# Kernel tuning notes

Hardware: AMD Instinct MI355X
Metric: run time of the kernel (lower is better)

## Reference

```python
import jax, jax.numpy as jnp
import numpy as np

DEPTH = 6


def sparsemax_last(z):
    # sparsemax along the last axis (Martins & Astudillo 2016)
    z_sorted = jnp.sort(z, axis=-1)[..., ::-1]
    k = jnp.arange(1, z.shape[-1] + 1, dtype=z.dtype)
    z_cum = jnp.cumsum(z_sorted, axis=-1)
    support = (1.0 + k * z_sorted) > z_cum
    k_z = jnp.sum(support, axis=-1, keepdims=True)  # number of support elems
    tau = (jnp.take_along_axis(z_cum, k_z.astype(jnp.int32) - 1, axis=-1) - 1.0) / k_z.astype(z.dtype)
    return jnp.maximum(z - tau, 0.0)


def binary_lookup_table(depth):
    # (depth, 2^depth, 2): bit d of leaf index c, stacked with its complement
    indices = np.arange(2 ** depth)
    offsets = 2 ** np.arange(depth)
    bits = (indices[None, :] // offsets[:, None]) % 2
    lut = np.stack([bits, 1 - bits], axis=-1).astype(np.float32)
    return jnp.asarray(lut)


def setup_inputs() -> dict:
    key = jax.random.key(0)
    k1, k2, k3 = jax.random.split(key, 3)
    batch, dim, n_trees, depth, units = 8192, 128, 512, DEPTH, 8
    inputs = jax.random.normal(k1, (batch, dim), dtype=jnp.float32)
    feature_selection_logits = jax.random.uniform(k2, (dim, n_trees, depth), dtype=jnp.float32)
    feature_thresholds = jnp.ones((n_trees, depth), dtype=jnp.float32)
    log_temperatures = jnp.ones((n_trees, depth), dtype=jnp.float32)
    response = jax.random.uniform(k3, (n_trees, units, 2 ** depth), dtype=jnp.float32)
    return {
        "inputs": inputs,
        "feature_selection_logits": feature_selection_logits,
        "feature_thresholds": feature_thresholds,
        "log_temperatures": log_temperatures,
        "response": response,
    }


def reference(inputs, feature_selection_logits, feature_thresholds, log_temperatures, response):
    depth = feature_thresholds.shape[-1]
    lut = binary_lookup_table(depth)  # (depth, C, 2)

    # sparsemax feature selection over the input-feature axis (dim)
    # logits: (dim, n, d) -> (n, d, dim)
    sel = sparsemax_last(jnp.transpose(feature_selection_logits, (1, 2, 0)))
    feature_values = jnp.einsum('bi,ndi->bnd', inputs, sel)  # (b, n, d)

    tl = (feature_values - feature_thresholds) * jnp.exp(-log_temperatures)
    gates = jnp.clip(0.5 * jnp.stack([-tl, tl], axis=-1) + 0.5, 0.0, 1.0)  # (b, n, d, 2)

    # leaf aggregation: prod over depth of per-level LUT contraction.
    # Loop over tiny depth axis to avoid materializing (b, n, d, 2^d).
    agg = None
    for i in range(depth):
        level = jnp.einsum('bns,cs->bnc', gates[:, :, i, :], lut[i])  # (b, n, C)
        agg = level if agg is None else agg * level

    out = jnp.einsum('bnc,nuc->bnu', agg, response)  # (b, n, units)
    return jnp.mean(out, axis=1)  # (b, units)
```

## Files before the change

### kernel.cpp

```cpp
#include <hip/hip_runtime.h>
#include <math.h>

#define BATCH  8192
#define DIM    128
#define NTREES 512
#define UNITS  8
#define RB 64
#define TB 64
#define NROWBLK (BATCH/RB)
#define NTREEBLK (NTREES/TB)

typedef __attribute__((ext_vector_type(8))) __bf16 bf16x8;
typedef __attribute__((ext_vector_type(4))) float f32x4;
typedef __attribute__((ext_vector_type(2))) float f32x2;
typedef __attribute__((ext_vector_type(4))) unsigned int u32x4;

static __device__ inline unsigned short f2bf(float v) {
  __bf16 h = (__bf16)v;
  return *(unsigned short*)&h;
}

static __device__ inline unsigned cvtpk(f32x2 v) {
  unsigned r;
  asm("v_cvt_pk_bf16_f32 %0, %1, %2" : "=v"(r) : "v"(v[0]), "v"(v[1]));
  return r;
}

__global__ __launch_bounds__(128) void prep_all(
    const float* __restrict__ logits, const float* __restrict__ thr,
    const float* __restrict__ logtemp, const float* __restrict__ inputs,
    const float* __restrict__ resp,
    unsigned short* __restrict__ Wfrag, unsigned short* __restrict__ Ximg,
    unsigned short* __restrict__ Rb, float* __restrict__ biasPad)
{
  const int b = blockIdx.x, tid = threadIdx.x;
  if (b < 4096) {
    const int t = b >> 3, d = b & 7;
    const int tb = t >> 6, sub = (t >> 4) & 3, w = (t >> 2) & 3, tq = t & 3;
    const int p = d >> 2, dloc = d & 3;
    const int ln = tq * 4 + dloc;
    const int S = (tb * 4 + sub) * 4 + w;
    const int ks = tid >> 5, G = (tid >> 3) & 3, j = tid & 7;
    const int lane = G * 16 + ln;
    const size_t wi = ((size_t)((S * 2 + p) * 4 + ks) * 64 + lane) * 8 + j;
    if (d >= 6) {
      Wfrag[wi] = 0;
      if (tid == 0) biasPad[t * 8 + d] = 0.f;
      return;
    }
    __shared__ __align__(16) float z[128];
    __shared__ float rc[128], rs[128];
    float zi = logits[((size_t)tid * NTREES + t) * 6 + d];
    z[tid] = zi;
    __syncthreads();
    float k = 0.f, Ssum = 0.f;
    const float4* z4 = (const float4*)z;
    #pragma unroll 4
    for (int q = 0; q < 32; ++q) {
      float4 v = z4[q];
      if (v.x >= zi) { k += 1.f; Ssum += v.x; }
      if (v.y >= zi) { k += 1.f; Ssum += v.y; }
      if (v.z >= zi) { k += 1.f; Ssum += v.z; }
      if (v.w >= zi) { k += 1.f; Ssum += v.w; }
    }
    bool sup = (1.f + k * zi) > Ssum;
    rc[tid] = sup ? 1.f : 0.f;
    rs[tid] = sup ? zi : 0.f;
    __syncthreads();
    for (int off = 64; off > 0; off >>= 1) {
      if (tid < off) { rc[tid] += rc[tid + off]; rs[tid] += rs[tid + off]; }
      __syncthreads();
    }
    float tau = (rs[0] - 1.f) / rc[0];
    float et = expf(-logtemp[t*6 + d]);
    Wfrag[wi] = f2bf(fmaxf(zi - tau, 0.f) * et);
    if (tid == 0) biasPad[t*8 + d] = -thr[t*6 + d] * et;
  } else if (b < 12288) {
    const int r = b - 4096;
    float v = inputs[(size_t)r * DIM + tid];
    int col = ((tid * 2) ^ ((r & 7) << 4)) >> 1;
    Ximg[(size_t)r * DIM + col] = f2bf(v);
  } else {
    const int idx = (b - 12288) * 128 + tid;
    const int j = idx & 7, lane = (idx >> 3) & 63;
    const int ks = (idx >> 9) & 3, half = (idx >> 11) & 1, S = idx >> 12;
    const int G = lane >> 4, u = lane & 15;
    const int tree = S * 4 + G;
    const int leaf = j | (ks << 3) | (half << 5);
    float v = (u < UNITS) ? resp[((size_t)tree*UNITS + u)*64 + leaf] : 0.f;
    Rb[idx] = f2bf(v);
  }
}

__global__ __launch_bounds__(256, 3) void odt_main(
    const unsigned short* __restrict__ Ximg, const unsigned short* __restrict__ Wfrag,
    const float* __restrict__ biasPad, const unsigned short* __restrict__ Rb,
    float* __restrict__ partial)
{
  __shared__ __align__(16) char pool[18432];
  char* Xl = pool;
  float* biasl = (float*)(pool + 16384);
  float* outred = (float*)pool;

  const int tid = threadIdx.x;
  const int lane = tid & 63;
  const int w = tid >> 6;
  const int G = lane >> 4;
  const int ln = lane & 15;

  const int wg = blockIdx.x;
  const int tb = wg & 7;
  const int bx = wg >> 3;

  {
    const float4* src = (const float4*)(Ximg + (size_t)bx * RB * DIM);
    float4* dst = (float4*)Xl;
    #pragma unroll
    for (int it = 0; it < 4; ++it) dst[tid + it * 256] = src[tid + it * 256];
  }
  biasl[tid]       = biasPad[(size_t)tb * 512 + tid];
  biasl[tid + 256] = biasPad[(size_t)tb * 512 + 256 + tid];
  __syncthreads();

  const char* xbase[4];
  #pragma unroll
  for (int ks = 0; ks < 4; ++ks)
    xbase[ks] = Xl + ln*256 + ((ks*64 + G*16) ^ ((ln & 7) << 4));

  f32x4 out[4];
  #pragma unroll
  for (int nt = 0; nt < 4; ++nt)
    #pragma unroll
    for (int r = 0; r < 4; ++r) out[nt][r] = 0.f;

  #pragma unroll 1
  for (int sub = 0; sub < 4; ++sub) {
    const int S = (tb*4 + sub)*4 + w;
    const bf16x8* wf = (const bf16x8*)Wfrag + (size_t)S * 8 * 64;
    const bf16x8* rb = (const bf16x8*)Rb   + (size_t)S * 8 * 64;
    bf16x8 Afr[2][4], B2[2][4];
    #pragma unroll
    for (int p = 0; p < 2; ++p)
      #pragma unroll
      for (int ks = 0; ks < 4; ++ks) {
        Afr[p][ks] = wf[(p*4 + ks)*64 + lane];
        B2[p][ks]  = rb[(p*4 + ks)*64 + lane];
      }
    const int tl8 = (sub*16 + w*4 + G) * 8;
    f32x2 bb[6];
    #pragma unroll
    for (int d = 0; d < 6; ++d) {
      float bvd = biasl[tl8 + d];
      bb[d] = (f32x2){0.5f + 0.5f*bvd, 0.5f - 0.5f*bvd};
    }

    #pragma unroll
    for (int nt = 0; nt < 4; ++nt) {
      bf16x8 Bfr[4];
      #pragma unroll
      for (int ks = 0; ks < 4; ++ks)
        Bfr[ks] = *(const bf16x8*)(xbase[ks] + nt*4096);
      f32x4 c1[2];
      #pragma unroll
      for (int p = 0; p < 2; ++p)
        #pragma unroll
        for (int r = 0; r < 4; ++r) c1[p][r] = 0.f;
      #pragma unroll
      for (int ks = 0; ks < 4; ++ks)
        c1[0] = __builtin_amdgcn_mfma_f32_16x16x32_bf16(Afr[0][ks], Bfr[ks], c1[0], 0,0,0);
      #pragma unroll
      for (int ks = 0; ks < 4; ++ks)
        c1[1] = __builtin_amdgcn_mfma_f32_16x16x32_bf16(Afr[1][ks], Bfr[ks], c1[1], 0,0,0);

      const f32x2 ch = (f32x2){0.5f, -0.5f};
      f32x2 P[6];
      #pragma unroll
      for (int d = 0; d < 6; ++d) {
        float fdv = (d < 4) ? c1[0][d] : c1[1][d-4];
        f32x2 t = fdv*ch + bb[d];
        P[d] = __builtin_elementwise_min(
                 __builtin_elementwise_max(t, (f32x2)0.f), (f32x2)1.f);
      }
      f32x2 qA = P[0]*P[1][0], qB = P[0]*P[1][1];
      f32x2 p3a = qA*P[2][0], p3b = qB*P[2][0];
      f32x2 p3c = qA*P[2][1], p3d = qB*P[2][1];
      f32x2 c34A = P[3]*P[4][0];
      f32x2 c34B = P[3]*P[4][1];

      #pragma unroll
      for (int h = 0; h < 2; ++h) {
        f32x2 ccA = c34A*P[5][h], ccB = c34B*P[5][h];
        float cc[4] = { ccA[0], ccA[1], ccB[0], ccB[1] };
        #pragma unroll
        for (int ks = 0; ks < 4; ++ks) {
          float c = cc[ks];
          u32x4 aw;
          aw[0] = cvtpk(p3a*c);
          aw[1] = cvtpk(p3b*c);
          aw[2] = cvtpk(p3c*c);
          aw[3] = cvtpk(p3d*c);
          bf16x8 A = __builtin_bit_cast(bf16x8, aw);
          out[nt] = __builtin_amdgcn_mfma_f32_16x16x32_bf16(A, B2[h][ks], out[nt], 0,0,0);
        }
      }
    }
  }

  __syncthreads();
  if (ln < UNITS) {
    #pragma unroll
    for (int nt = 0; nt < 4; ++nt)
      #pragma unroll
      for (int r = 0; r < 4; ++r)
        outred[((size_t)w*64 + nt*16 + 4*G + r)*8 + ln] = out[nt][r];
  }
  __syncthreads();
  #pragma unroll
  for (int v = 0; v < 2; ++v) {
    int e = tid + v*256;
    int row = e >> 3, u = e & 7;
    float sum = outred[(0*64 + row)*8 + u]
              + outred[(1*64 + row)*8 + u]
              + outred[(2*64 + row)*8 + u]
              + outred[(3*64 + row)*8 + u];
    partial[((size_t)tb*BATCH + bx*RB + row)*8 + u] = sum;
  }
}

__global__ __launch_bounds__(256) void odt_reduce(
    const f32x4* __restrict__ partial, f32x4* __restrict__ out)
{
  int i = blockIdx.x*256 + threadIdx.x;
  f32x4 sv;
  #pragma unroll
  for (int r = 0; r < 4; ++r) sv[r] = 0.f;
  #pragma unroll
  for (int t = 0; t < NTREEBLK; ++t) {
    f32x4 v = partial[(size_t)t * (BATCH*UNITS/4) + i];
    #pragma unroll
    for (int r = 0; r < 4; ++r) sv[r] += v[r];
  }
  #pragma unroll
  for (int r = 0; r < 4; ++r) sv[r] *= (1.f/NTREES);
  out[i] = sv;
}

extern "C" void kernel_launch(void* const* d_in, const int* in_sizes, int n_in,
                              void* d_out, int out_size, void* d_ws, size_t ws_size,
                              hipStream_t stream)
{
  const float* inputs   = (const float*)d_in[0];
  const float* logits   = (const float*)d_in[1];
  const float* thr      = (const float*)d_in[2];
  const float* logtemp  = (const float*)d_in[3];
  const float* response = (const float*)d_in[4];
  float* out = (float*)d_out;

  char* ws = (char*)d_ws;
  unsigned short* Wfrag = (unsigned short*)(ws);
  unsigned short* Ximg  = (unsigned short*)(ws + (1<<20));
  unsigned short* Rb    = (unsigned short*)(ws + (3<<20));
  float* biasPad        = (float*)(ws + (4<<20));
  float* partial        = (float*)(ws + (4<<20) + (1<<14));

  hipLaunchKernelGGL(prep_all, dim3(16384), dim3(128), 0, stream,
                     logits, thr, logtemp, inputs, response,
                     Wfrag, Ximg, Rb, biasPad);
  hipLaunchKernelGGL(odt_main, dim3(NROWBLK * NTREEBLK), dim3(256), 0, stream,
                     Ximg, Wfrag, biasPad, Rb, partial);
  hipLaunchKernelGGL(odt_reduce, dim3(BATCH * UNITS / 4 / 256), dim3(256), 0, stream,
                     (const f32x4*)partial, (f32x4*)out);
}
```

Measured before the change: 47.12 us.

## Split row tiles into two passes to cut registers and raise occupancy

The main kernel now processes the four 16-row tiles in two passes of two. Each pass keeps only two output accumulators and loads the response fragments later, which lowers live registers so launch bounds can target 4 waves per SIMD instead of 3. The cost is that the weight fragments and response fragments are reloaded from global memory twice per sub-block, plus an extra LDS reduction round per pass in a separate LDS region. Within each pass, the first-stage MFMAs for both tiles are grouped before the gating math, which gives the scheduler more overlap.

Result: slower. 48.34 us (+2.6%).

```diff
diff --git a/kernel.cpp b/kernel.cpp
--- a/kernel.cpp
+++ b/kernel.cpp
@@ -92,15 +92,15 @@
   }
 }
 
-__global__ __launch_bounds__(256, 3) void odt_main(
+__global__ __launch_bounds__(256, 4) void odt_main(
     const unsigned short* __restrict__ Ximg, const unsigned short* __restrict__ Wfrag,
     const float* __restrict__ biasPad, const unsigned short* __restrict__ Rb,
     float* __restrict__ partial)
 {
-  __shared__ __align__(16) char pool[18432];
+  __shared__ __align__(16) char pool[22528];
   char* Xl = pool;
   float* biasl = (float*)(pool + 16384);
-  float* outred = (float*)pool;
+  float* red   = (float*)(pool + 18432);
 
   const int tid = threadIdx.x;
   const int lane = tid & 63;
@@ -127,103 +127,114 @@
   for (int ks = 0; ks < 4; ++ks)
     xbase[ks] = Xl + ln*256 + ((ks*64 + G*16) ^ ((ln & 7) << 4));
 
-  f32x4 out[4];
-  #pragma unroll
-  for (int nt = 0; nt < 4; ++nt)
+  const f32x2 ch = (f32x2){0.5f, -0.5f};
+
+  #pragma unroll 1
+  for (int ntp = 0; ntp < 2; ++ntp) {
+    f32x4 out[2];
     #pragma unroll
-    for (int r = 0; r < 4; ++r) out[nt][r] = 0.f;
-
-  #pragma unroll 1
-  for (int sub = 0; sub < 4; ++sub) {
-    const int S = (tb*4 + sub)*4 + w;
-    const bf16x8* wf = (const bf16x8*)Wfrag + (size_t)S * 8 * 64;
-    const bf16x8* rb = (const bf16x8*)Rb   + (size_t)S * 8 * 64;
-    bf16x8 Afr[2][4], B2[2][4];
-    #pragma unroll
-    for (int p = 0; p < 2; ++p)
-      #pragma unroll
-      for (int ks = 0; ks < 4; ++ks) {
-        Afr[p][ks] = wf[(p*4 + ks)*64 + lane];
-        B2[p][ks]  = rb[(p*4 + ks)*64 + lane];
+    for (int n2 = 0; n2 < 2; ++n2)
+      #pragma unroll
+      for (int r = 0; r < 4; ++r) out[n2][r] = 0.f;
+
+    #pragma unroll 1
+    for (int sub = 0; sub < 4; ++sub) {
+      const int S = (tb*4 + sub)*4 + w;
+      const bf16x8* wf = (const bf16x8*)Wfrag + (size_t)S * 8 * 64;
+      const bf16x8* rb = (const bf16x8*)Rb   + (size_t)S * 8 * 64;
+
+      bf16x8 Afr[2][4];
+      #pragma unroll
+      for (int p = 0; p < 2; ++p)
+        #pragma unroll
+        for (int ks = 0; ks < 4; ++ks)
+          Afr[p][ks] = wf[(p*4 + ks)*64 + lane];
+
+      f32x4 c1[2][2];
+      #pragma unroll
+      for (int n2 = 0; n2 < 2; ++n2) {
+        const int nt = ntp*2 + n2;
+        bf16x8 Bfr[4];
+        #pragma unroll
+        for (int ks = 0; ks < 4; ++ks)
+          Bfr[ks] = *(const bf16x8*)(xbase[ks] + nt*4096);
+        #pragma unroll
+        for (int p = 0; p < 2; ++p)
+          #pragma unroll
+          for (int r = 0; r < 4; ++r) c1[n2][p][r] = 0.f;
+        #pragma unroll
+        for (int ks = 0; ks < 4; ++ks)
+          c1[n2][0] = __builtin_amdgcn_mfma_f32_16x16x32_bf16(Afr[0][ks], Bfr[ks], c1[n2][0], 0,0,0);
+        #pragma unroll
+        for (int ks = 0; ks < 4; ++ks)
+          c1[n2][1] = __builtin_amdgcn_mfma_f32_16x16x32_bf16(Afr[1][ks], Bfr[ks], c1[n2][1], 0,0,0);
       }
-    const int tl8 = (sub*16 + w*4 + G) * 8;
-    f32x2 bb[6];
-    #pragma unroll
-    for (int d = 0; d < 6; ++d) {
-      float bvd = biasl[tl8 + d];
-      bb[d] = (f32x2){0.5f + 0.5f*bvd, 0.5f - 0.5f*bvd};
-    }
-
-    #pragma unroll
-    for (int nt = 0; nt < 4; ++nt) {
-      bf16x8 Bfr[4];
-      #pragma unroll
-      for (int ks = 0; ks < 4; ++ks)
-        Bfr[ks] = *(const bf16x8*)(xbase[ks] + nt*4096);
-      f32x4 c1[2];
-      #pragma unroll
-      for (int p = 0; p < 2; ++p)
-        #pragma unroll
-        for (int r = 0; r < 4; ++r) c1[p][r] = 0.f;
-      #pragma unroll
-      for (int ks = 0; ks < 4; ++ks)
-        c1[0] = __builtin_amdgcn_mfma_f32_16x16x32_bf16(Afr[0][ks], Bfr[ks], c1[0], 0,0,0);
-      #pragma unroll
-      for (int ks = 0; ks < 4; ++ks)
-        c1[1] = __builtin_amdgcn_mfma_f32_16x16x32_bf16(Afr[1][ks], Bfr[ks], c1[1], 0,0,0);
-
-      const f32x2 ch = (f32x2){0.5f, -0.5f};
-      f32x2 P[6];
+
+      bf16x8 B2[2][4];
+      #pragma unroll
+      for (int h = 0; h < 2; ++h)
+        #pragma unroll
+        for (int ks = 0; ks < 4; ++ks)
+          B2[h][ks] = rb[(h*4 + ks)*64 + lane];
+
+      const int tl8 = (sub*16 + w*4 + G) * 8;
+      f32x2 bb[6];
       #pragma unroll
       for (int d = 0; d < 6; ++d) {
-        float fdv = (d < 4) ? c1[0][d] : c1[1][d-4];
-        f32x2 t = fdv*ch + bb[d];
-        P[d] = __builtin_elementwise_min(
-                 __builtin_elementwise_max(t, (f32x2)0.f), (f32x2)1.f);
+        float bvd = biasl[tl8 + d];
+        bb[d] = (f32x2){0.5f + 0.5f*bvd, 0.5f - 0.5f*bvd};
       }
-      f32x2 qA = P[0]*P[1][0], qB = P[0]*P[1][1];
-      f32x2 p3a = qA*P[2][0], p3b = qB*P[2][0];
-      f32x2 p3c = qA*P[2][1], p3d = qB*P[2][1];
-      f32x2 c34A = P[3]*P[4][0];
-      f32x2 c34B = P[3]*P[4][1];
-
-      #pragma unroll
-      for (int h = 0; h < 2; ++h) {
-        f32x2 ccA = c34A*P[5][h], ccB = c34B*P[5][h];
-        float cc[4] = { ccA[0], ccA[1], ccB[0], ccB[1] };
-        #pragma unroll
-        for (int ks = 0; ks < 4; ++ks) {
-          float c = cc[ks];
-          u32x4 aw;
-          aw[0] = cvtpk(p3a*c);
-          aw[1] = cvtpk(p3b*c);
-          aw[2] = cvtpk(p3c*c);
-          aw[3] = cvtpk(p3d*c);
-          bf16x8 A = __builtin_bit_cast(bf16x8, aw);
-          out[nt] = __builtin_amdgcn_mfma_f32_16x16x32_bf16(A, B2[h][ks], out[nt], 0,0,0);
+
+      #pragma unroll
+      for (int n2 = 0; n2 < 2; ++n2) {
+        f32x2 P[6];
+        #pragma unroll
+        for (int d = 0; d < 6; ++d) {
+          float fdv = (d < 4) ? c1[n2][0][d] : c1[n2][1][d-4];
+          f32x2 t = fdv*ch + bb[d];
+          P[d] = __builtin_elementwise_min(
+                   __builtin_elementwise_max(t, (f32x2)0.f), (f32x2)1.f);
+        }
+        f32x2 qA = P[0]*P[1][0], qB = P[0]*P[1][1];
+        f32x2 p3a = qA*P[2][0], p3b = qB*P[2][0];
+        f32x2 p3c = qA*P[2][1], p3d = qB*P[2][1];
+        f32x2 c34A = P[3]*P[4][0];
+        f32x2 c34B = P[3]*P[4][1];
+
+        #pragma unroll
+        for (int h = 0; h < 2; ++h) {
+          f32x2 ccA = c34A*P[5][h], ccB = c34B*P[5][h];
+          float cc[4] = { ccA[0], ccA[1], ccB[0], ccB[1] };
+          #pragma unroll
+          for (int ks = 0; ks < 4; ++ks) {
+            float c = cc[ks];
+            u32x4 aw;
+            aw[0] = cvtpk(p3a*c);
+            aw[1] = cvtpk(p3b*c);
+            aw[2] = cvtpk(p3c*c);
+            aw[3] = cvtpk(p3d*c);
+            bf16x8 A = __builtin_bit_cast(bf16x8, aw);
+            out[n2] = __builtin_amdgcn_mfma_f32_16x16x32_bf16(A, B2[h][ks], out[n2], 0,0,0);
+          }
         }
       }
     }
-  }
-
-  __syncthreads();
-  if (ln < UNITS) {
-    #pragma unroll
-    for (int nt = 0; nt < 4; ++nt)
-      #pragma unroll
-      for (int r = 0; r < 4; ++r)
-        outred[((size_t)w*64 + nt*16 + 4*G + r)*8 + ln] = out[nt][r];
-  }
-  __syncthreads();
-  #pragma unroll
-  for (int v = 0; v < 2; ++v) {
-    int e = tid + v*256;
-    int row = e >> 3, u = e & 7;
-    float sum = outred[(0*64 + row)*8 + u]
-              + outred[(1*64 + row)*8 + u]
-              + outred[(2*64 + row)*8 + u]
-              + outred[(3*64 + row)*8 + u];
-    partial[((size_t)tb*BATCH + bx*RB + row)*8 + u] = sum;
+
+    __syncthreads();
+    if (ln < UNITS) {
+      #pragma unroll
+      for (int n2 = 0; n2 < 2; ++n2)
+        #pragma unroll
+        for (int r = 0; r < 4; ++r)
+          red[w*256 + (n2*16 + 4*G + r)*8 + ln] = out[n2][r];
+    }
+    __syncthreads();
+    {
+      int row = tid >> 3, u = tid & 7;
+      float sum = red[0*256 + tid] + red[1*256 + tid]
+                + red[2*256 + tid] + red[3*256 + tid];
+      partial[((size_t)tb*BATCH + bx*RB + ntp*32 + row)*8 + u] = sum;
+    }
   }
 }
 
```

## Fuse input bf16 conversion into main kernel and compact padded weight/response fragments

Applied to the files above, without the earlier changes.

Drops the separate prep pass that converted inputs to a swizzled bf16 image. The main kernel now loads fp32 inputs directly, packs them to bf16 and writes the swizzled layout into LDS. The Wfrag and Rb fragment layouts are also compacted so the zero-padded depth rows and unused unit lanes are no longer written or stored, which shrinks the prep grid and the preprocessing traffic. In exchange, every odt_main workgroup re-reads fp32 inputs (twice the bytes of bf16) and converts them once per tree block, and the fragment loads use duplicated lane indexing.

Result: slower. 49.51 us (+5.1%).

```diff
diff --git a/kernel.cpp b/kernel.cpp
--- a/kernel.cpp
+++ b/kernel.cpp
@@ -9,11 +9,13 @@
 #define TB 64
 #define NROWBLK (BATCH/RB)
 #define NTREEBLK (NTREES/TB)
+#define WP1BASE 262144
 
 typedef __attribute__((ext_vector_type(8))) __bf16 bf16x8;
 typedef __attribute__((ext_vector_type(4))) float f32x4;
 typedef __attribute__((ext_vector_type(2))) float f32x2;
 typedef __attribute__((ext_vector_type(4))) unsigned int u32x4;
+typedef __attribute__((ext_vector_type(2))) unsigned int u32x2;
 
 static __device__ inline unsigned short f2bf(float v) {
   __bf16 h = (__bf16)v;
@@ -28,25 +30,23 @@
 
 __global__ __launch_bounds__(128) void prep_all(
     const float* __restrict__ logits, const float* __restrict__ thr,
-    const float* __restrict__ logtemp, const float* __restrict__ inputs,
-    const float* __restrict__ resp,
-    unsigned short* __restrict__ Wfrag, unsigned short* __restrict__ Ximg,
-    unsigned short* __restrict__ Rb, float* __restrict__ biasPad)
+    const float* __restrict__ logtemp, const float* __restrict__ resp,
+    unsigned short* __restrict__ Wfrag, unsigned short* __restrict__ Rb,
+    float* __restrict__ biasPad)
 {
   const int b = blockIdx.x, tid = threadIdx.x;
   if (b < 4096) {
     const int t = b >> 3, d = b & 7;
+    if (d >= 6) return;
     const int tb = t >> 6, sub = (t >> 4) & 3, w = (t >> 2) & 3, tq = t & 3;
-    const int p = d >> 2, dloc = d & 3;
-    const int ln = tq * 4 + dloc;
     const int S = (tb * 4 + sub) * 4 + w;
     const int ks = tid >> 5, G = (tid >> 3) & 3, j = tid & 7;
-    const int lane = G * 16 + ln;
-    const size_t wi = ((size_t)((S * 2 + p) * 4 + ks) * 64 + lane) * 8 + j;
-    if (d >= 6) {
-      Wfrag[wi] = 0;
-      if (tid == 0) biasPad[t * 8 + d] = 0.f;
-      return;
+    size_t wi;
+    if (d < 4) {
+      const int lane = G * 16 + tq * 4 + d;
+      wi = ((size_t)(S * 4 + ks) * 64 + lane) * 8 + j;
+    } else {
+      wi = WP1BASE + ((size_t)(S * 4 + ks) * 32 + G * 8 + tq * 2 + (d - 4)) * 8 + j;
     }
     __shared__ __align__(16) float z[128];
     __shared__ float rc[128], rs[128];
@@ -75,25 +75,20 @@
     float et = expf(-logtemp[t*6 + d]);
     Wfrag[wi] = f2bf(fmaxf(zi - tau, 0.f) * et);
     if (tid == 0) biasPad[t*8 + d] = -thr[t*6 + d] * et;
-  } else if (b < 12288) {
-    const int r = b - 4096;
-    float v = inputs[(size_t)r * DIM + tid];
-    int col = ((tid * 2) ^ ((r & 7) << 4)) >> 1;
-    Ximg[(size_t)r * DIM + col] = f2bf(v);
   } else {
-    const int idx = (b - 12288) * 128 + tid;
-    const int j = idx & 7, lane = (idx >> 3) & 63;
-    const int ks = (idx >> 9) & 3, half = (idx >> 11) & 1, S = idx >> 12;
-    const int G = lane >> 4, u = lane & 15;
+    const int idx2 = (b - 4096) * 128 + tid;
+    const int j = idx2 & 7, q = (idx2 >> 3) & 31;
+    const int G = q >> 3, u = q & 7;
+    const int frag = idx2 >> 8;
+    const int ks = frag & 3, h = (frag >> 2) & 1, S = frag >> 3;
     const int tree = S * 4 + G;
-    const int leaf = j | (ks << 3) | (half << 5);
-    float v = (u < UNITS) ? resp[((size_t)tree*UNITS + u)*64 + leaf] : 0.f;
-    Rb[idx] = f2bf(v);
+    const int leaf = j | (ks << 3) | (h << 5);
+    Rb[idx2] = f2bf(resp[((size_t)tree*UNITS + u)*64 + leaf]);
   }
 }
 
 __global__ __launch_bounds__(256, 3) void odt_main(
-    const unsigned short* __restrict__ Ximg, const unsigned short* __restrict__ Wfrag,
+    const float* __restrict__ inputs, const unsigned short* __restrict__ Wfrag,
     const float* __restrict__ biasPad, const unsigned short* __restrict__ Rb,
     float* __restrict__ partial)
 {
@@ -113,10 +108,18 @@
   const int bx = wg >> 3;
 
   {
-    const float4* src = (const float4*)(Ximg + (size_t)bx * RB * DIM);
-    float4* dst = (float4*)Xl;
-    #pragma unroll
-    for (int it = 0; it < 4; ++it) dst[tid + it * 256] = src[tid + it * 256];
+    const float4* src = (const float4*)(inputs + (size_t)bx * RB * DIM);
+    #pragma unroll
+    for (int it = 0; it < 8; ++it) {
+      int idx = tid + it * 256;
+      int row = idx >> 5, c4 = idx & 31;
+      float4 v = src[idx];
+      u32x2 pk;
+      pk[0] = cvtpk((f32x2){v.x, v.y});
+      pk[1] = cvtpk((f32x2){v.z, v.w});
+      int off = row * 256 + ((c4 * 8) ^ ((row & 7) << 4));
+      *(u32x2*)(Xl + off) = pk;
+    }
   }
   biasl[tid]       = biasPad[(size_t)tb * 512 + tid];
   biasl[tid + 256] = biasPad[(size_t)tb * 512 + 256 + tid];
@@ -133,19 +136,26 @@
     #pragma unroll
     for (int r = 0; r < 4; ++r) out[nt][r] = 0.f;
 
+  const f32x2 ch = (f32x2){0.5f, -0.5f};
+  const bf16x8* wp0 = (const bf16x8*)Wfrag;
+  const bf16x8* wp1 = (const bf16x8*)(Wfrag + WP1BASE);
+  const bf16x8* rbp = (const bf16x8*)Rb;
+
   #pragma unroll 1
   for (int sub = 0; sub < 4; ++sub) {
     const int S = (tb*4 + sub)*4 + w;
-    const bf16x8* wf = (const bf16x8*)Wfrag + (size_t)S * 8 * 64;
-    const bf16x8* rb = (const bf16x8*)Rb   + (size_t)S * 8 * 64;
     bf16x8 Afr[2][4], B2[2][4];
     #pragma unroll
-    for (int p = 0; p < 2; ++p)
-      #pragma unroll
-      for (int ks = 0; ks < 4; ++ks) {
-        Afr[p][ks] = wf[(p*4 + ks)*64 + lane];
-        B2[p][ks]  = rb[(p*4 + ks)*64 + lane];
-      }
+    for (int ks = 0; ks < 4; ++ks) {
+      Afr[0][ks] = wp0[(S*4 + ks)*64 + lane];
+      Afr[1][ks] = wp1[(S*4 + ks)*32 + G*8 + ((ln >> 2) << 1) + (ln & 1)];
+    }
+    #pragma unroll
+    for (int h = 0; h < 2; ++h)
+      #pragma unroll
+      for (int ks = 0; ks < 4; ++ks)
+        B2[h][ks] = rbp[(S*8 + h*4 + ks)*32 + G*8 + (ln & 7)];
+
     const int tl8 = (sub*16 + w*4 + G) * 8;
     f32x2 bb[6];
     #pragma unroll
@@ -172,7 +182,6 @@
       for (int ks = 0; ks < 4; ++ks)
         c1[1] = __builtin_amdgcn_mfma_f32_16x16x32_bf16(Afr[1][ks], Bfr[ks], c1[1], 0,0,0);
 
-      const f32x2 ch = (f32x2){0.5f, -0.5f};
       f32x2 P[6];
       #pragma unroll
       for (int d = 0; d < 6; ++d) {
@@ -258,16 +267,14 @@
 
   char* ws = (char*)d_ws;
   unsigned short* Wfrag = (unsigned short*)(ws);
-  unsigned short* Ximg  = (unsigned short*)(ws + (1<<20));
   unsigned short* Rb    = (unsigned short*)(ws + (3<<20));
   float* biasPad        = (float*)(ws + (4<<20));
   float* partial        = (float*)(ws + (4<<20) + (1<<14));
 
-  hipLaunchKernelGGL(prep_all, dim3(16384), dim3(128), 0, stream,
-                     logits, thr, logtemp, inputs, response,
-                     Wfrag, Ximg, Rb, biasPad);
+  hipLaunchKernelGGL(prep_all, dim3(6144), dim3(128), 0, stream,
+                     logits, thr, logtemp, response, Wfrag, Rb, biasPad);
   hipLaunchKernelGGL(odt_main, dim3(NROWBLK * NTREEBLK), dim3(256), 0, stream,
-                     Ximg, Wfrag, biasPad, Rb, partial);
+                     inputs, Wfrag, biasPad, Rb, partial);
   hipLaunchKernelGGL(odt_reduce, dim3(BATCH * UNITS / 4 / 256), dim3(256), 0, stream,
                      (const f32x4*)partial, (f32x4*)out);
 }
```

## Fuse final tree reduction into main kernel via last-block atomic counter

Applied to the files above, without the earlier changes.

Removes the separate odt_reduce launch. The last workgroup for each row group, detected through an atomic ticket counter that the prep kernel resets, sums the per-tree-block partials and writes the mean. It also changes the split: each workgroup now covers 128 rows (two row blocks) and 32 trees instead of 64 rows and 64 trees, so the grid has 1024 workgroups instead of 1024 at the old shape, and the weight and response fragments are reused across twice as many rows. The cost is a larger LDS footprint, more accumulator registers, and a serialized tail reduction run by one workgroup per group.

After: 98.45 us. +109.0%, slower.

```diff
diff --git a/kernel.cpp b/kernel.cpp
--- a/kernel.cpp
+++ b/kernel.cpp
@@ -6,9 +6,8 @@
 #define NTREES 512
 #define UNITS  8
 #define RB 64
-#define TB 64
-#define NROWBLK (BATCH/RB)
-#define NTREEBLK (NTREES/TB)
+#define NTB 16
+#define NBXG 64
 
 typedef __attribute__((ext_vector_type(8))) __bf16 bf16x8;
 typedef __attribute__((ext_vector_type(4))) float f32x4;
@@ -31,15 +30,15 @@
     const float* __restrict__ logtemp, const float* __restrict__ inputs,
     const float* __restrict__ resp,
     unsigned short* __restrict__ Wfrag, unsigned short* __restrict__ Ximg,
-    unsigned short* __restrict__ Rb, float* __restrict__ biasPad)
+    unsigned short* __restrict__ Rb, float* __restrict__ biasPad,
+    int* __restrict__ cnt)
 {
   const int b = blockIdx.x, tid = threadIdx.x;
   if (b < 4096) {
     const int t = b >> 3, d = b & 7;
-    const int tb = t >> 6, sub = (t >> 4) & 3, w = (t >> 2) & 3, tq = t & 3;
+    const int S = t >> 2, tq = t & 3;
     const int p = d >> 2, dloc = d & 3;
     const int ln = tq * 4 + dloc;
-    const int S = (tb * 4 + sub) * 4 + w;
     const int ks = tid >> 5, G = (tid >> 3) & 3, j = tid & 7;
     const int lane = G * 16 + ln;
     const size_t wi = ((size_t)((S * 2 + p) * 4 + ks) * 64 + lane) * 8 + j;
@@ -77,6 +76,7 @@
     if (tid == 0) biasPad[t*8 + d] = -thr[t*6 + d] * et;
   } else if (b < 12288) {
     const int r = b - 4096;
+    if (b == 4096 && tid < NBXG) cnt[tid] = 0;
     float v = inputs[(size_t)r * DIM + tid];
     int col = ((tid * 2) ^ ((r & 7) << 4)) >> 1;
     Ximg[(size_t)r * DIM + col] = f2bf(v);
@@ -95,12 +95,13 @@
 __global__ __launch_bounds__(256, 3) void odt_main(
     const unsigned short* __restrict__ Ximg, const unsigned short* __restrict__ Wfrag,
     const float* __restrict__ biasPad, const unsigned short* __restrict__ Rb,
-    float* __restrict__ partial)
+    float* __restrict__ partial, int* __restrict__ cnt, float* __restrict__ out)
 {
-  __shared__ __align__(16) char pool[18432];
+  __shared__ __align__(16) char pool[33808];
   char* Xl = pool;
-  float* biasl = (float*)(pool + 16384);
-  float* outred = (float*)pool;
+  float* biasl = (float*)(pool + 32768);
+  int* tick    = (int*)(pool + 33792);
+  float* red   = (float*)pool;
 
   const int tid = threadIdx.x;
   const int lane = tid & 63;
@@ -109,17 +110,17 @@
   const int ln = lane & 15;
 
   const int wg = blockIdx.x;
-  const int tb = wg & 7;
-  const int bx = wg >> 3;
+  const int tb  = (wg & 7) * 2 + ((wg >> 3) & 1);
+  const int bxg = wg >> 4;
+  const int bx0 = bxg * 2;
 
   {
-    const float4* src = (const float4*)(Ximg + (size_t)bx * RB * DIM);
+    const float4* src = (const float4*)(Ximg + (size_t)bx0 * RB * DIM);
     float4* dst = (float4*)Xl;
     #pragma unroll
-    for (int it = 0; it < 4; ++it) dst[tid + it * 256] = src[tid + it * 256];
-  }
-  biasl[tid]       = biasPad[(size_t)tb * 512 + tid];
-  biasl[tid + 256] = biasPad[(size_t)tb * 512 + 256 + tid];
+    for (int it = 0; it < 8; ++it) dst[tid + it * 256] = src[tid + it * 256];
+  }
+  biasl[tid & 255] = biasPad[(size_t)tb * 256 + (tid & 255)];
   __syncthreads();
 
   const char* xbase[4];
@@ -127,15 +128,19 @@
   for (int ks = 0; ks < 4; ++ks)
     xbase[ks] = Xl + ln*256 + ((ks*64 + G*16) ^ ((ln & 7) << 4));
 
-  f32x4 out[4];
+  f32x4 out_[2][4];
   #pragma unroll
-  for (int nt = 0; nt < 4; ++nt)
-    #pragma unroll
-    for (int r = 0; r < 4; ++r) out[nt][r] = 0.f;
+  for (int bxq = 0; bxq < 2; ++bxq)
+    #pragma unroll
+    for (int nt = 0; nt < 4; ++nt)
+      #pragma unroll
+      for (int r = 0; r < 4; ++r) out_[bxq][nt][r] = 0.f;
+
+  const f32x2 ch = (f32x2){0.5f, -0.5f};
 
   #pragma unroll 1
-  for (int sub = 0; sub < 4; ++sub) {
-    const int S = (tb*4 + sub)*4 + w;
+  for (int sub = 0; sub < 2; ++sub) {
+    const int S = tb*8 + sub*4 + w;
     const bf16x8* wf = (const bf16x8*)Wfrag + (size_t)S * 8 * 64;
     const bf16x8* rb = (const bf16x8*)Rb   + (size_t)S * 8 * 64;
     bf16x8 Afr[2][4], B2[2][4];
@@ -146,7 +151,7 @@
         Afr[p][ks] = wf[(p*4 + ks)*64 + lane];
         B2[p][ks]  = rb[(p*4 + ks)*64 + lane];
       }
-    const int tl8 = (sub*16 + w*4 + G) * 8;
+    const int tl8 = ((sub*4 + w)*4 + G) * 8;
     f32x2 bb[6];
     #pragma unroll
     for (int d = 0; d < 6; ++d) {
@@ -155,94 +160,98 @@
     }
 
     #pragma unroll
-    for (int nt = 0; nt < 4; ++nt) {
-      bf16x8 Bfr[4];
-      #pragma unroll
-      for (int ks = 0; ks < 4; ++ks)
-        Bfr[ks] = *(const bf16x8*)(xbase[ks] + nt*4096);
-      f32x4 c1[2];
-      #pragma unroll
-      for (int p = 0; p < 2; ++p)
-        #pragma unroll
-        for (int r = 0; r < 4; ++r) c1[p][r] = 0.f;
-      #pragma unroll
-      for (int ks = 0; ks < 4; ++ks)
-        c1[0] = __builtin_amdgcn_mfma_f32_16x16x32_bf16(Afr[0][ks], Bfr[ks], c1[0], 0,0,0);
-      #pragma unroll
-      for (int ks = 0; ks < 4; ++ks)
-        c1[1] = __builtin_amdgcn_mfma_f32_16x16x32_bf16(Afr[1][ks], Bfr[ks], c1[1], 0,0,0);
-
-      const f32x2 ch = (f32x2){0.5f, -0.5f};
-      f32x2 P[6];
-      #pragma unroll
-      for (int d = 0; d < 6; ++d) {
-        float fdv = (d < 4) ? c1[0][d] : c1[1][d-4];
-        f32x2 t = fdv*ch + bb[d];
-        P[d] = __builtin_elementwise_min(
-                 __builtin_elementwise_max(t, (f32x2)0.f), (f32x2)1.f);
-      }
-      f32x2 qA = P[0]*P[1][0], qB = P[0]*P[1][1];
-      f32x2 p3a = qA*P[2][0], p3b = qB*P[2][0];
-      f32x2 p3c = qA*P[2][1], p3d = qB*P[2][1];
-      f32x2 c34A = P[3]*P[4][0];
-      f32x2 c34B = P[3]*P[4][1];
-
-      #pragma unroll
-      for (int h = 0; h < 2; ++h) {
-        f32x2 ccA = c34A*P[5][h], ccB = c34B*P[5][h];
-        float cc[4] = { ccA[0], ccA[1], ccB[0], ccB[1] };
-        #pragma unroll
-        for (int ks = 0; ks < 4; ++ks) {
-          float c = cc[ks];
-          u32x4 aw;
-          aw[0] = cvtpk(p3a*c);
-          aw[1] = cvtpk(p3b*c);
-          aw[2] = cvtpk(p3c*c);
-          aw[3] = cvtpk(p3d*c);
-          bf16x8 A = __builtin_bit_cast(bf16x8, aw);
-          out[nt] = __builtin_amdgcn_mfma_f32_16x16x32_bf16(A, B2[h][ks], out[nt], 0,0,0);
+    for (int bxq = 0; bxq < 2; ++bxq) {
+      #pragma unroll
+      for (int nt = 0; nt < 4; ++nt) {
+        bf16x8 Bfr[4];
+        #pragma unroll
+        for (int ks = 0; ks < 4; ++ks)
+          Bfr[ks] = *(const bf16x8*)(xbase[ks] + bxq*16384 + nt*4096);
+        f32x4 c1[2];
+        #pragma unroll
+        for (int p = 0; p < 2; ++p)
+          #pragma unroll
+          for (int r = 0; r < 4; ++r) c1[p][r] = 0.f;
+        #pragma unroll
+        for (int ks = 0; ks < 4; ++ks)
+          c1[0] = __builtin_amdgcn_mfma_f32_16x16x32_bf16(Afr[0][ks], Bfr[ks], c1[0], 0,0,0);
+        #pragma unroll
+        for (int ks = 0; ks < 4; ++ks)
+          c1[1] = __builtin_amdgcn_mfma_f32_16x16x32_bf16(Afr[1][ks], Bfr[ks], c1[1], 0,0,0);
+
+        f32x2 P[6];
+        #pragma unroll
+        for (int d = 0; d < 6; ++d) {
+          float fdv = (d < 4) ? c1[0][d] : c1[1][d-4];
+          f32x2 t = fdv*ch + bb[d];
+          P[d] = __builtin_elementwise_min(
+                   __builtin_elementwise_max(t, (f32x2)0.f), (f32x2)1.f);
+        }
+        f32x2 qA = P[0]*P[1][0], qB = P[0]*P[1][1];
+        f32x2 p3a = qA*P[2][0], p3b = qB*P[2][0];
+        f32x2 p3c = qA*P[2][1], p3d = qB*P[2][1];
+        f32x2 c34A = P[3]*P[4][0];
+        f32x2 c34B = P[3]*P[4][1];
+
+        #pragma unroll
+        for (int h = 0; h < 2; ++h) {
+          f32x2 ccA = c34A*P[5][h], ccB = c34B*P[5][h];
+          float cc[4] = { ccA[0], ccA[1], ccB[0], ccB[1] };
+          #pragma unroll
+          for (int ks = 0; ks < 4; ++ks) {
+            float c = cc[ks];
+            u32x4 aw;
+            aw[0] = cvtpk(p3a*c);
+            aw[1] = cvtpk(p3b*c);
+            aw[2] = cvtpk(p3c*c);
+            aw[3] = cvtpk(p3d*c);
+            bf16x8 A = __builtin_bit_cast(bf16x8, aw);
+            out_[bxq][nt] = __builtin_amdgcn_mfma_f32_16x16x32_bf16(A, B2[h][ks], out_[bxq][nt], 0,0,0);
+          }
         }
       }
     }
   }
 
+  #pragma unroll
+  for (int bxq = 0; bxq < 2; ++bxq) {
+    __syncthreads();
+    if (ln < UNITS) {
+      #pragma unroll
+      for (int nt = 0; nt < 4; ++nt)
+        #pragma unroll
+        for (int r = 0; r < 4; ++r)
+          red[w*512 + (nt*16 + 4*G + r)*8 + ln] = out_[bxq][nt][r];
+    }
+    __syncthreads();
+    #pragma unroll
+    for (int v = 0; v < 2; ++v) {
+      int e = tid + v*256;
+      float sum = red[0*512 + e] + red[1*512 + e]
+                + red[2*512 + e] + red[3*512 + e];
+      partial[((size_t)tb*128 + bx0 + bxq)*512 + e] = sum;
+    }
+  }
+
   __syncthreads();
-  if (ln < UNITS) {
-    #pragma unroll
-    for (int nt = 0; nt < 4; ++nt)
-      #pragma unroll
-      for (int r = 0; r < 4; ++r)
-        outred[((size_t)w*64 + nt*16 + 4*G + r)*8 + ln] = out[nt][r];
+  if (tid == 0) {
+    __threadfence();
+    *tick = atomicAdd(&cnt[bxg], 1);
   }
   __syncthreads();
-  #pragma unroll
-  for (int v = 0; v < 2; ++v) {
-    int e = tid + v*256;
-    int row = e >> 3, u = e & 7;
-    float sum = outred[(0*64 + row)*8 + u]
-              + outred[(1*64 + row)*8 + u]
-              + outred[(2*64 + row)*8 + u]
-              + outred[(3*64 + row)*8 + u];
-    partial[((size_t)tb*BATCH + bx*RB + row)*8 + u] = sum;
-  }
-}
-
-__global__ __launch_bounds__(256) void odt_reduce(
-    const f32x4* __restrict__ partial, f32x4* __restrict__ out)
-{
-  int i = blockIdx.x*256 + threadIdx.x;
-  f32x4 sv;
-  #pragma unroll
-  for (int r = 0; r < 4; ++r) sv[r] = 0.f;
-  #pragma unroll
-  for (int t = 0; t < NTREEBLK; ++t) {
-    f32x4 v = partial[(size_t)t * (BATCH*UNITS/4) + i];
-    #pragma unroll
-    for (int r = 0; r < 4; ++r) sv[r] += v[r];
-  }
-  #pragma unroll
-  for (int r = 0; r < 4; ++r) sv[r] *= (1.f/NTREES);
-  out[i] = sv;
+  if (*tick == NTB - 1) {
+    __threadfence();
+    #pragma unroll
+    for (int v = 0; v < 4; ++v) {
+      int e = tid + v*256;
+      int bx = bx0 + (e >> 9), re = e & 511;
+      float sum = 0.f;
+      #pragma unroll
+      for (int t16 = 0; t16 < NTB; ++t16)
+        sum += partial[((size_t)t16*128 + bx)*512 + re];
+      out[(size_t)bx*512 + re] = sum * (1.f/NTREES);
+    }
+  }
 }
 
 extern "C" void kernel_launch(void* const* d_in, const int* in_sizes, int n_in,
@@ -261,13 +270,12 @@
   unsigned short* Ximg  = (unsigned short*)(ws + (1<<20));
   unsigned short* Rb    = (unsigned short*)(ws + (3<<20));
   float* biasPad        = (float*)(ws + (4<<20));
-  float* partial        = (float*)(ws + (4<<20) + (1<<14));
+  int* cnt              = (int*)(ws + (4<<20) + (1<<14));
+  float* partial        = (float*)(ws + (4<<20) + (1<<15));
 
   hipLaunchKernelGGL(prep_all, dim3(16384), dim3(128), 0, stream,
                      logits, thr, logtemp, inputs, response,
-                     Wfrag, Ximg, Rb, biasPad);
-  hipLaunchKernelGGL(odt_main, dim3(NROWBLK * NTREEBLK), dim3(256), 0, stream,
-                     Ximg, Wfrag, biasPad, Rb, partial);
-  hipLaunchKernelGGL(odt_reduce, dim3(BATCH * UNITS / 4 / 256), dim3(256), 0, stream,
-                     (const f32x4*)partial, (f32x4*)out);
-}
+                     Wfrag, Ximg, Rb, biasPad, cnt);
+  hipLaunchKernelGGL(odt_main, dim3(NTB * NBXG), dim3(256), 0, stream,
+                     Ximg, Wfrag, biasPad, Rb, partial, cnt, out);
+}
```
